# Kernel tuning notes

Hardware: AMD Instinct MI355X
Metric: run time of the kernel (lower is better)

The kernel has to match this reference:

```python
import jax, jax.numpy as jnp
import numpy as np

B, N, C, H = 64, 500, 128, 256
EPS = 1e-5


def _bn(x, g, b):
    # BatchNorm1d in training mode: biased batch statistics
    m = jnp.mean(x, axis=0)
    v = jnp.mean((x - m) ** 2, axis=0)
    return g * (x - m) * jax.lax.rsqrt(v + EPS) + b


def _lin(x, w, b):
    return x @ w.T + b


def setup_inputs() -> dict:
    key = jax.random.key(0)
    ks = jax.random.split(key, 16)

    def w(k, shape, s=0.05):
        return (s * jax.random.normal(k, shape)).astype(jnp.float32)

    return {
        'l2_xyz': jax.random.uniform(ks[0], (B, 3, N), dtype=jnp.float32),
        'l2_points': jax.random.normal(ks[1], (B, C, N), dtype=jnp.float32),
        'l3_points': jax.random.normal(ks[2], (B, C), dtype=jnp.float32),
        'temp': jax.random.uniform(ks[3], (B, 1, N), dtype=jnp.float32) * 400.0,
        'fc_res0_w': w(ks[4], (H, H)), 'fc_res0_b': jnp.zeros((H,), jnp.float32),
        'bn_res0_g': jnp.ones((H,), jnp.float32), 'bn_res0_b': jnp.zeros((H,), jnp.float32),
        'fc_res1_w': w(ks[5], (H, H)), 'fc_res1_b': jnp.zeros((H,), jnp.float32),
        'bn_res1_g': jnp.ones((H,), jnp.float32), 'bn_res1_b': jnp.zeros((H,), jnp.float32),
        'fc_res2_w': w(ks[6], (H, H)), 'fc_res2_b': jnp.zeros((H,), jnp.float32),
        'bn_res2_g': jnp.ones((H,), jnp.float32), 'bn_res2_b': jnp.zeros((H,), jnp.float32),
        'fc_lt1_w': w(ks[7], (H, H)), 'fc_lt1_b': jnp.zeros((H,), jnp.float32),
        'bn_lt1_g': jnp.ones((H,), jnp.float32), 'bn_lt1_b': jnp.zeros((H,), jnp.float32),
        'fc_lt4_w': w(ks[8], (1, H)), 'fc_lt4_b': jnp.zeros((1,), jnp.float32),
    }


def reference(l2_xyz, l2_points, l3_points, temp,
              fc_res0_w, fc_res0_b, bn_res0_g, bn_res0_b,
              fc_res1_w, fc_res1_b, bn_res1_g, bn_res1_b,
              fc_res2_w, fc_res2_b, bn_res2_g, bn_res2_b,
              fc_lt1_w, fc_lt1_b, bn_lt1_g, bn_lt1_b,
              fc_lt4_w, fc_lt4_b):
    point = jnp.transpose(l2_xyz, (0, 2, 1))    # [B,N,3]
    data = jnp.transpose(l2_points, (0, 2, 1))  # [B,N,C]

    # square_distance(point, point), then abs + sqrt
    s = jnp.sum(point * point, axis=-1)  # [B,N]
    sq = s[:, :, None] + s[:, None, :] - 2.0 * jnp.einsum('bik,bjk->bij', point, point)
    dist = jnp.sqrt(jnp.abs(sq))  # [B,N,N]

    # distance-band edge set as a mask (torch.where -> variable edge list)
    mask = ((dist > 0.19) & (dist < 0.21)).astype(data.dtype)  # [B,N,N]
    counts = jnp.maximum(jnp.sum(mask, axis=(1, 2)), 1.0)      # [B] edges per batch

    # per-channel average of data[b,i,c]*data[b,j,c] over edges (b,i,j).
    # Identical math to the torch take/index_add channel loop over corr_matrix,
    # without materializing the [B,C,N,N] outer-product tensor.
    t = jnp.einsum('bij,bjc->bic', mask, data)                  # [B,N,C]
    correlation = jnp.einsum('bic,bic->bc', t, data) / counts[:, None]  # [B,C]

    sa4 = l3_points.reshape(B, C)
    c = jnp.concatenate([correlation, sa4], axis=1)  # [B,256]

    h = jax.nn.relu(_bn(_lin(c, fc_res0_w, fc_res0_b), bn_res0_g, bn_res0_b))
    h = jax.nn.relu(_bn(_lin(h, fc_res1_w, fc_res1_b), bn_res1_g, bn_res1_b))
    h = jax.nn.relu(_bn(_lin(h, fc_res2_w, fc_res2_b), bn_res2_g, bn_res2_b))
    h = jax.nn.relu(_bn(_lin(h, fc_lt1_w, fc_lt1_b), bn_lt1_g, bn_lt1_b))
    tc = _lin(h, fc_lt4_w, fc_lt4_b).squeeze(-1)  # [B]

    tsys = jnp.mean(temp, axis=2).squeeze(-1)     # [B]
    return (tc, tsys, l2_points, correlation)
```

## Files before the change

kernel.cpp:

```cpp
#include <hip/hip_runtime.h>

#define NB 64
#define NP 500
#define NC 128
#define NH 256
#define EPS_BN 1e-5f

#define SEGS 8
#define CAPE 1024

#define EDGE_OFF 0
#define EDGE_WORDS (NB * SEGS * CAPE)
#define CNT_OFF (EDGE_OFF + EDGE_WORDS)
#define CT_OFF (CNT_OFF + 512)
#define H1_OFF (CT_OFF + NH * NB)
#define H2_OFF (H1_OFF + NH * NB)

#define OUT_PTS_OFF 128
#define OUT_CORR_OFF 4096128

#define COPY_BLKS 768
#define TOTAL_F4 1024000

__global__ __launch_bounds__(256) void k1_scan_misc_copy(
    const float* __restrict__ xyz,
    const float* __restrict__ temp,
    const float* __restrict__ l3,
    const float* __restrict__ b4,
    const float* __restrict__ pts,
    float* __restrict__ out,
    float* __restrict__ ws) {
  const int blk = blockIdx.x;
  const int tid = threadIdx.x;

  if (blk < 512) {
    const int b = blk >> 3;
    const int jt = blk & 7;
    __shared__ float4 pt[NP];
    __shared__ int lcnt;
    if (tid == 0) lcnt = 0;
    const float* xr = xyz + b * 1500;
    for (int idx = tid; idx < NP; idx += 256) {
      float x = xr[idx], y = xr[500 + idx], z = xr[1000 + idx];
      float s = x * x + y * y + z * z;
      pt[idx] = make_float4(x, y, z, s);
    }
    __syncthreads();

    const int j0 = jt * 63;
    const int j1 = (j0 + 63 < NP) ? j0 + 63 : NP;
    const int i0 = tid;
    const int i1 = tid + 256;
    float4 p0 = pt[i0];
    float4 p1 = (i1 < NP) ? pt[i1] : make_float4(0.f, 0.f, 0.f, 0.f);
    int* eseg = (int*)ws + EDGE_OFF + (b * SEGS + jt) * CAPE;

    for (int j = j0; j < j1; ++j) {
      float4 q = pt[j];
      if (i0 < j) {
        float dot = p0.x * q.x + p0.y * q.y + p0.z * q.z;
        float sq = p0.w + q.w - 2.f * dot;
        float d = sqrtf(fabsf(sq));
        if (d > 0.19f && d < 0.21f) {
          int e = atomicAdd(&lcnt, 1);
          if (e < CAPE) eseg[e] = (i0 << 16) | j;
        }
      }
      if (i1 < j) {
        float dot = p1.x * q.x + p1.y * q.y + p1.z * q.z;
        float sq = p1.w + q.w - 2.f * dot;
        float d = sqrtf(fabsf(sq));
        if (d > 0.19f && d < 0.21f) {
          int e = atomicAdd(&lcnt, 1);
          if (e < CAPE) eseg[e] = (i1 << 16) | j;
        }
      }
    }
    __syncthreads();
    if (tid == 0) {
      int c = lcnt < CAPE ? lcnt : CAPE;
      ((int*)ws)[CNT_OFF + b * SEGS + jt] = c;
    }
  } else if (blk < 576) {
    const int b = blk - 512;
    float sum = 0.f;
    for (int i = tid; i < NP; i += 256) sum += temp[b * NP + i];
    for (int off = 32; off; off >>= 1) sum += __shfl_xor(sum, off);
    __shared__ float wsum[4];
    if ((tid & 63) == 0) wsum[tid >> 6] = sum;
    __syncthreads();
    if (tid == 0)
      out[64 + b] = (wsum[0] + wsum[1] + wsum[2] + wsum[3]) * (1.f / 500.f);
    if (tid < 128) ws[CT_OFF + (128 + tid) * 64 + b] = l3[b * NC + tid];
    if (tid == 0) out[b] = b4[0];
  } else {
    const int cb = blk - 576;
    const float4* src = (const float4*)pts;
    float4* dst = (float4*)(out + OUT_PTS_OFF);
    for (int idx = cb * 256 + tid; idx < TOTAL_F4 / 2; idx += COPY_BLKS * 256)
      dst[idx] = src[idx];
  }
}

__global__ __launch_bounds__(256) void k2_corr_copy(
    const float* __restrict__ data,
    float* __restrict__ out,
    float* __restrict__ ws) {
  const int blk = blockIdx.x;
  const int tid = threadIdx.x;

  if (blk < 512) {
    const int b = blk >> 3;
    const int c0 = (blk & 7) * 16;
    __shared__ float dT[NP * 20];
    __shared__ float corrp[16];
    if (tid < 16) corrp[tid] = 0.f;

    const float4* in4 = (const float4*)(data + (size_t)b * 64000 + c0 * 500);
    for (int idx = tid; idx < 2000; idx += 256) {
      float4 v = in4[idx];
      int c = idx / 125;
      int j = (idx - c * 125) * 4;
      dT[(j + 0) * 20 + c] = v.x;
      dT[(j + 1) * 20 + c] = v.y;
      dT[(j + 2) * 20 + c] = v.z;
      dT[(j + 3) * 20 + c] = v.w;
    }
    __syncthreads();

    const int quad = tid & 3;
    const int slot = tid >> 2;
    float4 acc = make_float4(0.f, 0.f, 0.f, 0.f);
    const int* cnts = (const int*)ws + CNT_OFF + b * SEGS;
    int Etot = 0;
    for (int seg = 0; seg < SEGS; ++seg) {
      int E = cnts[seg];
      Etot += E;
      const int* eseg = (const int*)ws + EDGE_OFF + (b * SEGS + seg) * CAPE;
      for (int e = slot; e < E; e += 64) {
        int ij = eseg[e];
        int i = ij >> 16, j = ij & 0xffff;
        const float4 a = *(const float4*)(dT + i * 20 + quad * 4);
        const float4 c4 = *(const float4*)(dT + j * 20 + quad * 4);
        acc.x += a.x * c4.x;
        acc.y += a.y * c4.y;
        acc.z += a.z * c4.z;
        acc.w += a.w * c4.w;
      }
    }
    for (int off = 4; off < 64; off <<= 1) {
      acc.x += __shfl_xor(acc.x, off);
      acc.y += __shfl_xor(acc.y, off);
      acc.z += __shfl_xor(acc.z, off);
      acc.w += __shfl_xor(acc.w, off);
    }
    if ((tid & 63) < 4) {
      atomicAdd(&corrp[quad * 4 + 0], acc.x);
      atomicAdd(&corrp[quad * 4 + 1], acc.y);
      atomicAdd(&corrp[quad * 4 + 2], acc.z);
      atomicAdd(&corrp[quad * 4 + 3], acc.w);
    }
    __syncthreads();
    if (tid < 16) {
      float denom = fmaxf(2.f * (float)Etot, 1.f);
      float v = 2.f * corrp[tid] / denom;
      out[OUT_CORR_OFF + b * NC + c0 + tid] = v;
      ws[CT_OFF + (c0 + tid) * 64 + b] = v;
    }
  } else {
    const int cb = blk - 512;
    const float4* src = (const float4*)data;
    float4* dst = (float4*)(out + OUT_PTS_OFF);
    for (int idx = TOTAL_F4 / 2 + cb * 256 + tid; idx < TOTAL_F4;
         idx += COPY_BLKS * 256)
      dst[idx] = src[idx];
  }
}

__global__ __launch_bounds__(256) void layer_k(
    const float* __restrict__ xT, const float* __restrict__ W,
    const float* __restrict__ bias, const float* __restrict__ g,
    const float* __restrict__ be, float* __restrict__ yT,
    const float* __restrict__ w4, float* __restrict__ tc) {
  const int o = blockIdx.x;
  const int b = threadIdx.x & 63;
  const int w = threadIdx.x >> 6;
  const float* wr = W + o * NH + w * 64;
  const float* xp = xT + (w * 64) * 64 + b;
  float acc = 0.f;
#pragma unroll
  for (int i = 0; i < 64; ++i) acc += xp[i * 64] * wr[i];
  __shared__ float part[4][64];
  part[w][b] = acc;
  __syncthreads();
  if (w == 0) {
    float t = part[0][b] + part[1][b] + part[2][b] + part[3][b] + bias[o];
    float s1 = t;
    for (int off = 32; off; off >>= 1) s1 += __shfl_xor(s1, off);
    float m = s1 * (1.f / 64.f);
    float d = t - m;
    float s2 = d * d;
    for (int off = 32; off; off >>= 1) s2 += __shfl_xor(s2, off);
    float var = s2 * (1.f / 64.f);
    float h = g[o] * d * rsqrtf(var + EPS_BN) + be[o];
    h = fmaxf(h, 0.f);
    if (w4) {
      atomicAdd(&tc[b], w4[o] * h);
    } else {
      yT[o * 64 + b] = h;
    }
  }
}

extern "C" void kernel_launch(void* const* d_in, const int* in_sizes, int n_in,
                              void* d_out, int out_size, void* d_ws,
                              size_t ws_size, hipStream_t stream) {
  const float* xyz = (const float*)d_in[0];
  const float* pts = (const float*)d_in[1];
  const float* l3 = (const float*)d_in[2];
  const float* temp = (const float*)d_in[3];
  const float* w0 = (const float*)d_in[4];
  const float* b0 = (const float*)d_in[5];
  const float* g0 = (const float*)d_in[6];
  const float* be0 = (const float*)d_in[7];
  const float* w1 = (const float*)d_in[8];
  const float* b1 = (const float*)d_in[9];
  const float* g1 = (const float*)d_in[10];
  const float* be1 = (const float*)d_in[11];
  const float* w2 = (const float*)d_in[12];
  const float* b2 = (const float*)d_in[13];
  const float* g2 = (const float*)d_in[14];
  const float* be2 = (const float*)d_in[15];
  const float* w3 = (const float*)d_in[16];
  const float* b3 = (const float*)d_in[17];
  const float* g3 = (const float*)d_in[18];
  const float* be3 = (const float*)d_in[19];
  const float* w4 = (const float*)d_in[20];
  const float* b4 = (const float*)d_in[21];

  float* out = (float*)d_out;
  float* ws = (float*)d_ws;
  float* cT = ws + CT_OFF;
  float* hA = ws + H1_OFF;
  float* hB = ws + H2_OFF;

  k1_scan_misc_copy<<<576 + COPY_BLKS, 256, 0, stream>>>(xyz, temp, l3, b4,
                                                         pts, out, ws);
  k2_corr_copy<<<512 + COPY_BLKS, 256, 0, stream>>>(pts, out, ws);
  layer_k<<<256, 256, 0, stream>>>(cT, w0, b0, g0, be0, hA, nullptr, nullptr);
  layer_k<<<256, 256, 0, stream>>>(hA, w1, b1, g1, be1, hB, nullptr, nullptr);
  layer_k<<<256, 256, 0, stream>>>(hB, w2, b2, g2, be2, hA, nullptr, nullptr);
  layer_k<<<256, 256, 0, stream>>>(hA, w3, b3, g3, be3, nullptr, w4, out);
}
```

Baseline: 164.8 us.

## Fuse correlation and MLP layers into one cooperative kernel with grid syncs

The correlation stage and the four MLP layers now run in one cooperative kernel of 512 blocks, with grid.sync() between layers instead of five separate launches. The whole l2_points copy moves into the first kernel, which now has 1024 copy blocks. The aim is to remove launch gaps and tail effects between the small layer kernels. In exchange, grid-wide barriers add their own cost, the first kernel now carries the full copy, and the cooperative launch needs all 512 blocks co-resident while each holds about 40KB of shared memory.

```diff
diff --git a/kernel.cpp b/kernel.cpp
--- a/kernel.cpp
+++ b/kernel.cpp
@@ -1,4 +1,7 @@
 #include <hip/hip_runtime.h>
+#include <hip/hip_cooperative_groups.h>
+
+namespace cg = cooperative_groups;
 
 #define NB 64
 #define NP 500
@@ -19,7 +22,7 @@
 #define OUT_PTS_OFF 128
 #define OUT_CORR_OFF 4096128
 
-#define COPY_BLKS 768
+#define COPY_BLKS 1024
 #define TOTAL_F4 1024000
 
 __global__ __launch_bounds__(256) void k1_scan_misc_copy(
@@ -97,26 +100,38 @@
     const int cb = blk - 576;
     const float4* src = (const float4*)pts;
     float4* dst = (float4*)(out + OUT_PTS_OFF);
-    for (int idx = cb * 256 + tid; idx < TOTAL_F4 / 2; idx += COPY_BLKS * 256)
+    for (int idx = cb * 256 + tid; idx < TOTAL_F4; idx += COPY_BLKS * 256)
       dst[idx] = src[idx];
   }
 }
 
-__global__ __launch_bounds__(256) void k2_corr_copy(
-    const float* __restrict__ data,
-    float* __restrict__ out,
-    float* __restrict__ ws) {
+struct P2 {
+  const float* data;
+  const float* W0; const float* B0; const float* G0; const float* E0;
+  const float* W1; const float* B1; const float* G1; const float* E1;
+  const float* W2; const float* B2; const float* G2; const float* E2;
+  const float* W3; const float* B3; const float* G3; const float* E3;
+  const float* w4;
+  float* out;
+  float* ws;
+};
+
+__global__ __launch_bounds__(256) void k2_mega(P2 p) {
+  cg::grid_group grid = cg::this_grid();
   const int blk = blockIdx.x;
   const int tid = threadIdx.x;
-
-  if (blk < 512) {
+  float* ws = p.ws;
+
+  __shared__ float dT[NP * 20];
+  __shared__ float corrp[16];
+  __shared__ float part[4][64];
+
+  {
     const int b = blk >> 3;
     const int c0 = (blk & 7) * 16;
-    __shared__ float dT[NP * 20];
-    __shared__ float corrp[16];
     if (tid < 16) corrp[tid] = 0.f;
 
-    const float4* in4 = (const float4*)(data + (size_t)b * 64000 + c0 * 500);
+    const float4* in4 = (const float4*)(p.data + (size_t)b * 64000 + c0 * 500);
     for (int idx = tid; idx < 2000; idx += 256) {
       float4 v = in4[idx];
       int c = idx / 125;
@@ -164,50 +179,51 @@
     if (tid < 16) {
       float denom = fmaxf(2.f * (float)Etot, 1.f);
       float v = 2.f * corrp[tid] / denom;
-      out[OUT_CORR_OFF + b * NC + c0 + tid] = v;
+      p.out[OUT_CORR_OFF + b * NC + c0 + tid] = v;
       ws[CT_OFF + (c0 + tid) * 64 + b] = v;
     }
-  } else {
-    const int cb = blk - 512;
-    const float4* src = (const float4*)data;
-    float4* dst = (float4*)(out + OUT_PTS_OFF);
-    for (int idx = TOTAL_F4 / 2 + cb * 256 + tid; idx < TOTAL_F4;
-         idx += COPY_BLKS * 256)
-      dst[idx] = src[idx];
   }
-}
-
-__global__ __launch_bounds__(256) void layer_k(
-    const float* __restrict__ xT, const float* __restrict__ W,
-    const float* __restrict__ bias, const float* __restrict__ g,
-    const float* __restrict__ be, float* __restrict__ yT,
-    const float* __restrict__ w4, float* __restrict__ tc) {
-  const int o = blockIdx.x;
-  const int b = threadIdx.x & 63;
-  const int w = threadIdx.x >> 6;
-  const float* wr = W + o * NH + w * 64;
-  const float* xp = xT + (w * 64) * 64 + b;
-  float acc = 0.f;
+
+  float* cT = ws + CT_OFF;
+  float* hA = ws + H1_OFF;
+  float* hB = ws + H2_OFF;
+  const float* Ws[4] = {p.W0, p.W1, p.W2, p.W3};
+  const float* Bs[4] = {p.B0, p.B1, p.B2, p.B3};
+  const float* Gs[4] = {p.G0, p.G1, p.G2, p.G3};
+  const float* Es[4] = {p.E0, p.E1, p.E2, p.E3};
+  const float* xs[4] = {cT, hA, hB, hA};
+  float* ys[4] = {hA, hB, hA, nullptr};
+
+  for (int l = 0; l < 4; ++l) {
+    grid.sync();
+    if (blk < 256) {
+      const int o = blk;
+      const int b = tid & 63;
+      const int w = tid >> 6;
+      const float* wr = Ws[l] + o * NH + w * 64;
+      const float* xp = xs[l] + (w * 64) * 64 + b;
+      float acc = 0.f;
 #pragma unroll
-  for (int i = 0; i < 64; ++i) acc += xp[i * 64] * wr[i];
-  __shared__ float part[4][64];
-  part[w][b] = acc;
-  __syncthreads();
-  if (w == 0) {
-    float t = part[0][b] + part[1][b] + part[2][b] + part[3][b] + bias[o];
-    float s1 = t;
-    for (int off = 32; off; off >>= 1) s1 += __shfl_xor(s1, off);
-    float m = s1 * (1.f / 64.f);
-    float d = t - m;
-    float s2 = d * d;
-    for (int off = 32; off; off >>= 1) s2 += __shfl_xor(s2, off);
-    float var = s2 * (1.f / 64.f);
-    float h = g[o] * d * rsqrtf(var + EPS_BN) + be[o];
-    h = fmaxf(h, 0.f);
-    if (w4) {
-      atomicAdd(&tc[b], w4[o] * h);
-    } else {
-      yT[o * 64 + b] = h;
+      for (int i = 0; i < 64; ++i) acc += xp[i * 64] * wr[i];
+      part[w][b] = acc;
+      __syncthreads();
+      if (w == 0) {
+        float t = part[0][b] + part[1][b] + part[2][b] + part[3][b] + Bs[l][o];
+        float s1 = t;
+        for (int off = 32; off; off >>= 1) s1 += __shfl_xor(s1, off);
+        float m = s1 * (1.f / 64.f);
+        float d = t - m;
+        float s2 = d * d;
+        for (int off = 32; off; off >>= 1) s2 += __shfl_xor(s2, off);
+        float var = s2 * (1.f / 64.f);
+        float h = Gs[l][o] * d * rsqrtf(var + EPS_BN) + Es[l][o];
+        h = fmaxf(h, 0.f);
+        if (l == 3) {
+          atomicAdd(&p.out[b], p.w4[o] * h);
+        } else {
+          ys[l][o * 64 + b] = h;
+        }
+      }
     }
   }
 }
@@ -219,36 +235,28 @@
   const float* pts = (const float*)d_in[1];
   const float* l3 = (const float*)d_in[2];
   const float* temp = (const float*)d_in[3];
-  const float* w0 = (const float*)d_in[4];
-  const float* b0 = (const float*)d_in[5];
-  const float* g0 = (const float*)d_in[6];
-  const float* be0 = (const float*)d_in[7];
-  const float* w1 = (const float*)d_in[8];
-  const float* b1 = (const float*)d_in[9];
-  const float* g1 = (const float*)d_in[10];
-  const float* be1 = (const float*)d_in[11];
-  const float* w2 = (const float*)d_in[12];
-  const float* b2 = (const float*)d_in[13];
-  const float* g2 = (const float*)d_in[14];
-  const float* be2 = (const float*)d_in[15];
-  const float* w3 = (const float*)d_in[16];
-  const float* b3 = (const float*)d_in[17];
-  const float* g3 = (const float*)d_in[18];
-  const float* be3 = (const float*)d_in[19];
-  const float* w4 = (const float*)d_in[20];
-  const float* b4 = (const float*)d_in[21];
 
   float* out = (float*)d_out;
   float* ws = (float*)d_ws;
-  float* cT = ws + CT_OFF;
-  float* hA = ws + H1_OFF;
-  float* hB = ws + H2_OFF;
-
-  k1_scan_misc_copy<<<576 + COPY_BLKS, 256, 0, stream>>>(xyz, temp, l3, b4,
-                                                         pts, out, ws);
-  k2_corr_copy<<<512 + COPY_BLKS, 256, 0, stream>>>(pts, out, ws);
-  layer_k<<<256, 256, 0, stream>>>(cT, w0, b0, g0, be0, hA, nullptr, nullptr);
-  layer_k<<<256, 256, 0, stream>>>(hA, w1, b1, g1, be1, hB, nullptr, nullptr);
-  layer_k<<<256, 256, 0, stream>>>(hB, w2, b2, g2, be2, hA, nullptr, nullptr);
-  layer_k<<<256, 256, 0, stream>>>(hA, w3, b3, g3, be3, nullptr, w4, out);
+
+  k1_scan_misc_copy<<<576 + COPY_BLKS, 256, 0, stream>>>(
+      xyz, temp, l3, (const float*)d_in[21], pts, out, ws);
+
+  P2 p;
+  p.data = pts;
+  p.W0 = (const float*)d_in[4];  p.B0 = (const float*)d_in[5];
+  p.G0 = (const float*)d_in[6];  p.E0 = (const float*)d_in[7];
+  p.W1 = (const float*)d_in[8];  p.B1 = (const float*)d_in[9];
+  p.G1 = (const float*)d_in[10]; p.E1 = (const float*)d_in[11];
+  p.W2 = (const float*)d_in[12]; p.B2 = (const float*)d_in[13];
+  p.G2 = (const float*)d_in[14]; p.E2 = (const float*)d_in[15];
+  p.W3 = (const float*)d_in[16]; p.B3 = (const float*)d_in[17];
+  p.G3 = (const float*)d_in[18]; p.E3 = (const float*)d_in[19];
+  p.w4 = (const float*)d_in[20];
+  p.out = out;
+  p.ws = ws;
+
+  void* args[] = {&p};
+  hipLaunchCooperativeKernel(reinterpret_cast<void*>(k2_mega), dim3(512),
+                             dim3(256), args, 0, stream);
 }
```

Measured after the change: 416.2 us. 2.53x slower.

## Fuse edge scan and correlation into one kernel with shared-memory edge list

Applied to the files above, without the earlier changes.

Merges the pair-scan kernel and the correlation kernel into a single launch. Each block now scans all point pairs for one batch, keeps the edge list in shared memory and accumulates correlation for 16 channels directly. The global edge buffer round-trip and one launch go away, and the data tile is stored channel-major instead of transposed. In exchange, the O(N^2) pair scan is repeated 8 times per batch (once per channel group), and the larger LDS footprint may lower occupancy. The copy blocks are interleaved with the compute blocks.

```diff
diff --git a/kernel.cpp b/kernel.cpp
--- a/kernel.cpp
+++ b/kernel.cpp
@@ -6,174 +6,134 @@
 #define NH 256
 #define EPS_BN 1e-5f
 
-#define SEGS 8
-#define CAPE 1024
-
-#define EDGE_OFF 0
-#define EDGE_WORDS (NB * SEGS * CAPE)
-#define CNT_OFF (EDGE_OFF + EDGE_WORDS)
-#define CT_OFF (CNT_OFF + 512)
-#define H1_OFF (CT_OFF + NH * NB)
-#define H2_OFF (H1_OFF + NH * NB)
+#define ECAP 4096
+
+#define CT_OFF 0
+#define H1_OFF (NH * NB)
+#define H2_OFF (2 * NH * NB)
 
 #define OUT_PTS_OFF 128
 #define OUT_CORR_OFF 4096128
 
-#define COPY_BLKS 768
-#define TOTAL_F4 1024000
-
-__global__ __launch_bounds__(256) void k1_scan_misc_copy(
+
+#define CHK(P, I, Q, J)                                     \
+  if ((I) < (J)) {                                          \
+    float dot_ = P.x * Q.x + P.y * Q.y + P.z * Q.z;         \
+    float d_ = sqrtf(fabsf(P.w + Q.w - 2.f * dot_));        \
+    if (d_ > 0.19f && d_ < 0.21f) {                         \
+      int e_ = atomicAdd(&lcnt, 1);                         \
+      if (e_ < ECAP) sm.c.eL[e_] = ((I) << 16) | (J);       \
+    }                                                       \
+  }
+
+__global__ __launch_bounds__(256) void k1(
     const float* __restrict__ xyz,
+    const float* __restrict__ data,
+    const float* __restrict__ l3,
     const float* __restrict__ temp,
-    const float* __restrict__ l3,
     const float* __restrict__ b4,
-    const float* __restrict__ pts,
     float* __restrict__ out,
     float* __restrict__ ws) {
   const int blk = blockIdx.x;
   const int tid = threadIdx.x;
 
-  if (blk < 512) {
-    const int b = blk >> 3;
-    const int jt = blk & 7;
-    __shared__ float4 pt[NP];
-    __shared__ int lcnt;
+  __shared__ union {
+    struct {
+      float4 pt[NP];
+      int eL[ECAP];
+      float dT[16 * 504];
+      float corrp[16];
+    } c;
+    struct { float wsum[4]; } m;
+  } sm;
+  __shared__ int lcnt;
+
+  if (blk < 1024) {
+    const int role = blk & 1;
+    const int id = blk >> 1;
+    if (role == 1) {
+      const float4* src = (const float4*)data;
+      float4* dst = (float4*)(out + OUT_PTS_OFF);
+      for (int idx = id * 256 + tid; idx < 1024000; idx += 512 * 256)
+        dst[idx] = src[idx];
+      return;
+    }
+    const int b = id >> 3;
+    const int c0 = (id & 7) * 16;
     if (tid == 0) lcnt = 0;
+    if (tid < 16) sm.c.corrp[tid] = 0.f;
+
     const float* xr = xyz + b * 1500;
     for (int idx = tid; idx < NP; idx += 256) {
       float x = xr[idx], y = xr[500 + idx], z = xr[1000 + idx];
-      float s = x * x + y * y + z * z;
-      pt[idx] = make_float4(x, y, z, s);
-    }
-    __syncthreads();
-
-    const int j0 = jt * 63;
-    const int j1 = (j0 + 63 < NP) ? j0 + 63 : NP;
-    const int i0 = tid;
-    const int i1 = tid + 256;
-    float4 p0 = pt[i0];
-    float4 p1 = (i1 < NP) ? pt[i1] : make_float4(0.f, 0.f, 0.f, 0.f);
-    int* eseg = (int*)ws + EDGE_OFF + (b * SEGS + jt) * CAPE;
-
-    for (int j = j0; j < j1; ++j) {
-      float4 q = pt[j];
-      if (i0 < j) {
-        float dot = p0.x * q.x + p0.y * q.y + p0.z * q.z;
-        float sq = p0.w + q.w - 2.f * dot;
-        float d = sqrtf(fabsf(sq));
-        if (d > 0.19f && d < 0.21f) {
-          int e = atomicAdd(&lcnt, 1);
-          if (e < CAPE) eseg[e] = (i0 << 16) | j;
-        }
+      sm.c.pt[idx] = make_float4(x, y, z, x * x + y * y + z * z);
+    }
+    const float4* in4 = (const float4*)data + b * 16000 + c0 * 125;
+    for (int k = tid; k < 2000; k += 256) {
+      float4 v = in4[k];
+      int c = k / 125;
+      int j4 = k - c * 125;
+      *(float4*)(&sm.c.dT[c * 504 + 4 * j4]) = v;
+    }
+    __syncthreads();
+
+    {
+      const int i0 = tid, i1 = tid + 256;
+      float4 p0 = sm.c.pt[i0];
+      float4 p1 = (i1 < NP) ? sm.c.pt[i1] : make_float4(0.f, 0.f, 0.f, 0.f);
+#pragma unroll 4
+      for (int j = 1; j < NP; ++j) {
+        float4 q = sm.c.pt[j];
+        CHK(p0, i0, q, j)
+        CHK(p1, i1, q, j)
       }
-      if (i1 < j) {
-        float dot = p1.x * q.x + p1.y * q.y + p1.z * q.z;
-        float sq = p1.w + q.w - 2.f * dot;
-        float d = sqrtf(fabsf(sq));
-        if (d > 0.19f && d < 0.21f) {
-          int e = atomicAdd(&lcnt, 1);
-          if (e < CAPE) eseg[e] = (i1 << 16) | j;
-        }
-      }
-    }
-    __syncthreads();
-    if (tid == 0) {
-      int c = lcnt < CAPE ? lcnt : CAPE;
-      ((int*)ws)[CNT_OFF + b * SEGS + jt] = c;
-    }
-  } else if (blk < 576) {
-    const int b = blk - 512;
-    float sum = 0.f;
-    for (int i = tid; i < NP; i += 256) sum += temp[b * NP + i];
-    for (int off = 32; off; off >>= 1) sum += __shfl_xor(sum, off);
-    __shared__ float wsum[4];
-    if ((tid & 63) == 0) wsum[tid >> 6] = sum;
+    }
+    __syncthreads();
+
+    const int E = lcnt < ECAP ? lcnt : ECAP;
+    const int quad = tid & 3;
+    const int slot = tid >> 2;
+    float a0 = 0.f, a1 = 0.f, a2 = 0.f, a3 = 0.f;
+    const float* Cb = sm.c.dT + quad * 4 * 504;
+    for (int e = slot; e < E; e += 64) {
+      int ij = sm.c.eL[e];
+      int i = ij >> 16, j = ij & 0xffff;
+      a0 += Cb[i] * Cb[j];
+      a1 += Cb[504 + i] * Cb[504 + j];
+      a2 += Cb[1008 + i] * Cb[1008 + j];
+      a3 += Cb[1512 + i] * Cb[1512 + j];
+    }
+    for (int off = 4; off < 64; off <<= 1) {
+      a0 += __shfl_xor(a0, off);
+      a1 += __shfl_xor(a1, off);
+      a2 += __shfl_xor(a2, off);
+      a3 += __shfl_xor(a3, off);
+    }
+    if ((tid & 63) < 4) {
+      atomicAdd(&sm.c.corrp[quad * 4 + 0], a0);
+      atomicAdd(&sm.c.corrp[quad * 4 + 1], a1);
+      atomicAdd(&sm.c.corrp[quad * 4 + 2], a2);
+      atomicAdd(&sm.c.corrp[quad * 4 + 3], a3);
+    }
+    __syncthreads();
+    if (tid < 16) {
+      float denom = fmaxf(2.f * (float)lcnt, 1.f);
+      float v = 2.f * sm.c.corrp[tid] / denom;
+      out[OUT_CORR_OFF + b * NC + c0 + tid] = v;
+      ws[CT_OFF + (c0 + tid) * 64 + b] = v;
+    }
+  } else {
+    const int b = blk - 1024;
+    float s = 0.f;
+    for (int i = tid; i < NP; i += 256) s += temp[b * NP + i];
+    for (int off = 32; off; off >>= 1) s += __shfl_xor(s, off);
+    if ((tid & 63) == 0) sm.m.wsum[tid >> 6] = s;
     __syncthreads();
     if (tid == 0)
-      out[64 + b] = (wsum[0] + wsum[1] + wsum[2] + wsum[3]) * (1.f / 500.f);
+      out[64 + b] = (sm.m.wsum[0] + sm.m.wsum[1] + sm.m.wsum[2] +
+                     sm.m.wsum[3]) * (1.f / 500.f);
     if (tid < 128) ws[CT_OFF + (128 + tid) * 64 + b] = l3[b * NC + tid];
     if (tid == 0) out[b] = b4[0];
-  } else {
-    const int cb = blk - 576;
-    const float4* src = (const float4*)pts;
-    float4* dst = (float4*)(out + OUT_PTS_OFF);
-    for (int idx = cb * 256 + tid; idx < TOTAL_F4 / 2; idx += COPY_BLKS * 256)
-      dst[idx] = src[idx];
-  }
-}
-
-__global__ __launch_bounds__(256) void k2_corr_copy(
-    const float* __restrict__ data,
-    float* __restrict__ out,
-    float* __restrict__ ws) {
-  const int blk = blockIdx.x;
-  const int tid = threadIdx.x;
-
-  if (blk < 512) {
-    const int b = blk >> 3;
-    const int c0 = (blk & 7) * 16;
-    __shared__ float dT[NP * 20];
-    __shared__ float corrp[16];
-    if (tid < 16) corrp[tid] = 0.f;
-
-    const float4* in4 = (const float4*)(data + (size_t)b * 64000 + c0 * 500);
-    for (int idx = tid; idx < 2000; idx += 256) {
-      float4 v = in4[idx];
-      int c = idx / 125;
-      int j = (idx - c * 125) * 4;
-      dT[(j + 0) * 20 + c] = v.x;
-      dT[(j + 1) * 20 + c] = v.y;
-      dT[(j + 2) * 20 + c] = v.z;
-      dT[(j + 3) * 20 + c] = v.w;
-    }
-    __syncthreads();
-
-    const int quad = tid & 3;
-    const int slot = tid >> 2;
-    float4 acc = make_float4(0.f, 0.f, 0.f, 0.f);
-    const int* cnts = (const int*)ws + CNT_OFF + b * SEGS;
-    int Etot = 0;
-    for (int seg = 0; seg < SEGS; ++seg) {
-      int E = cnts[seg];
-      Etot += E;
-      const int* eseg = (const int*)ws + EDGE_OFF + (b * SEGS + seg) * CAPE;
-      for (int e = slot; e < E; e += 64) {
-        int ij = eseg[e];
-        int i = ij >> 16, j = ij & 0xffff;
-        const float4 a = *(const float4*)(dT + i * 20 + quad * 4);
-        const float4 c4 = *(const float4*)(dT + j * 20 + quad * 4);
-        acc.x += a.x * c4.x;
-        acc.y += a.y * c4.y;
-        acc.z += a.z * c4.z;
-        acc.w += a.w * c4.w;
-      }
-    }
-    for (int off = 4; off < 64; off <<= 1) {
-      acc.x += __shfl_xor(acc.x, off);
-      acc.y += __shfl_xor(acc.y, off);
-      acc.z += __shfl_xor(acc.z, off);
-      acc.w += __shfl_xor(acc.w, off);
-    }
-    if ((tid & 63) < 4) {
-      atomicAdd(&corrp[quad * 4 + 0], acc.x);
-      atomicAdd(&corrp[quad * 4 + 1], acc.y);
-      atomicAdd(&corrp[quad * 4 + 2], acc.z);
-      atomicAdd(&corrp[quad * 4 + 3], acc.w);
-    }
-    __syncthreads();
-    if (tid < 16) {
-      float denom = fmaxf(2.f * (float)Etot, 1.f);
-      float v = 2.f * corrp[tid] / denom;
-      out[OUT_CORR_OFF + b * NC + c0 + tid] = v;
-      ws[CT_OFF + (c0 + tid) * 64 + b] = v;
-    }
-  } else {
-    const int cb = blk - 512;
-    const float4* src = (const float4*)data;
-    float4* dst = (float4*)(out + OUT_PTS_OFF);
-    for (int idx = TOTAL_F4 / 2 + cb * 256 + tid; idx < TOTAL_F4;
-         idx += COPY_BLKS * 256)
-      dst[idx] = src[idx];
   }
 }
 
@@ -244,9 +204,7 @@
   float* hA = ws + H1_OFF;
   float* hB = ws + H2_OFF;
 
-  k1_scan_misc_copy<<<576 + COPY_BLKS, 256, 0, stream>>>(xyz, temp, l3, b4,
-                                                         pts, out, ws);
-  k2_corr_copy<<<512 + COPY_BLKS, 256, 0, stream>>>(pts, out, ws);
+  k1<<<1088, 256, 0, stream>>>(xyz, pts, l3, temp, b4, out, ws);
   layer_k<<<256, 256, 0, stream>>>(cT, w0, b0, g0, be0, hA, nullptr, nullptr);
   layer_k<<<256, 256, 0, stream>>>(hA, w1, b1, g1, be1, hB, nullptr, nullptr);
   layer_k<<<256, 256, 0, stream>>>(hB, w2, b2, g2, be2, hA, nullptr, nullptr);
```

After: 382.9 us. 132% more time.
